# Optimization experiments

Measured on AMD Instinct MI355X. Metric: run time of the kernel, lower is better.

Reference implementation:

```python
import jax, jax.numpy as jnp
import numpy as np


def setup_inputs() -> dict:
    key = jax.random.key(0)
    ks = jax.random.split(key, 11)
    B, T, H1, H2 = 256, 512, 1024, 1024
    s1 = 1.0 / np.sqrt(H1)
    s2 = 1.0 / np.sqrt(H2)
    return {
        "x": jax.random.normal(ks[0], (B, 2, T), dtype=jnp.float32),
        "W_ih1": jax.random.normal(ks[1], (H1, 2), dtype=jnp.float32) * s1,
        "W_hh1": jax.random.normal(ks[2], (H1, H1), dtype=jnp.float32) * s1,
        "b_ih1": jax.random.normal(ks[3], (H1,), dtype=jnp.float32) * s1,
        "b_hh1": jax.random.normal(ks[4], (H1,), dtype=jnp.float32) * s1,
        "W_ih2": jax.random.normal(ks[5], (H2, H1), dtype=jnp.float32) * s2,
        "W_hh2": jax.random.normal(ks[6], (H2, H2), dtype=jnp.float32) * s2,
        "b_ih2": jax.random.normal(ks[7], (H2,), dtype=jnp.float32) * s2,
        "b_hh2": jax.random.normal(ks[8], (H2,), dtype=jnp.float32) * s2,
        "W_lin": jax.random.normal(ks[9], (2, H2), dtype=jnp.float32) * s2,
        "b_lin": jax.random.normal(ks[10], (2,), dtype=jnp.float32) * s2,
        "future": 0,
    }


def _run(x, W_ih1, W_hh1, b_ih1, b_hh1, W_ih2, W_hh2, b_ih2, b_hh2, W_lin, b_lin, future):
    # x: [B, 2, T]  -> scan over time with xs [T, B, 2]
    B = x.shape[0]
    H1, H2 = W_hh1.shape[0], W_hh2.shape[0]

    def cell(x_t, h1, h2):
        # torch RNNCell (tanh): h' = tanh(x W_ih^T + b_ih + h W_hh^T + b_hh)
        h1 = jnp.tanh(x_t @ W_ih1.T + b_ih1 + h1 @ W_hh1.T + b_hh1)
        h2 = jnp.tanh(h1 @ W_ih2.T + b_ih2 + h2 @ W_hh2.T + b_hh2)
        out = h2 @ W_lin.T + b_lin  # [B, 2]
        return h1, h2, out

    def step(carry, x_t):
        h1, h2 = carry
        h1, h2, out = cell(x_t, h1, h2)
        return (h1, h2), out

    h1 = jnp.zeros((B, H1), dtype=x.dtype)
    h2 = jnp.zeros((B, H2), dtype=x.dtype)
    xs = jnp.transpose(x, (2, 0, 1))  # [T, B, 2]
    (h1, h2), outs = jax.lax.scan(step, (h1, h2), xs)  # outs: [T, B, 2]

    if future > 0:
        last = outs[-1]

        def fstep(carry, _):
            h1, h2, out = carry
            h1, h2, out = cell(out, h1, h2)
            return (h1, h2, out), out

        _, fouts = jax.lax.scan(fstep, (h1, h2, last), None, length=future)
        outs = jnp.concatenate([outs, fouts], axis=0)

    return jnp.transpose(outs, (1, 2, 0))  # [B, 2, T+future]


def reference(x, W_ih1, W_hh1, b_ih1, b_hh1, W_ih2, W_hh2, b_ih2, b_hh2, W_lin, b_lin, future):
    return _run(x, W_ih1, W_hh1, b_ih1, b_hh1, W_ih2, W_hh2, b_ih2, b_hh2, W_lin, b_lin, future)
```

## Files before the change

### kernel.cpp

```cpp
#include <hip/hip_runtime.h>

#define NB 256
#define NT 512
#define NH 1024
#define BH (NB * NH)
#define GRID_WGS 256
#define BLOCK 512

typedef __attribute__((ext_vector_type(8))) __bf16 bfrag;
typedef __attribute__((ext_vector_type(4))) float f32x4;
typedef __attribute__((ext_vector_type(4))) unsigned u32x4;
typedef __attribute__((ext_vector_type(8))) unsigned short u16x8;
typedef unsigned short us;

__device__ __attribute__((aligned(16))) us g_h1[3 * BH];
__device__ __attribute__((aligned(16))) us g_h2[4 * BH];
__device__ __attribute__((aligned(128))) unsigned g_flagA[GRID_WGS];
__device__ __attribute__((aligned(128))) unsigned g_flagB[GRID_WGS];

__device__ __forceinline__ us f2bf(float f) {
  union { float f; unsigned u; } v; v.f = f;
  unsigned r = v.u + 0x7FFFu + ((v.u >> 16) & 1u);
  return (us)(r >> 16);
}
__device__ __forceinline__ float bf2f(us u) {
  union { unsigned u; float f; } v; v.u = ((unsigned)u) << 16;
  return v.f;
}

__device__ __forceinline__ bfrag cvt8(const float* __restrict__ p) {
  f32x4 a = *reinterpret_cast<const f32x4*>(p);
  f32x4 b = *reinterpret_cast<const f32x4*>(p + 4);
  u16x8 u;
#pragma unroll
  for (int i = 0; i < 4; ++i) { u[i] = f2bf(a[i]); u[i + 4] = f2bf(b[i]); }
  union { u16x8 u; bfrag b; } c; c.u = u; return c.b;
}

union f16u { u32x4 v; bfrag b; u16x8 s; };
__device__ __forceinline__ u32x4 ld16_dev(const void* p) {
  u32x4 r;
  asm volatile("global_load_dwordx4 %0, %1, off sc0 sc1" : "=v"(r) : "v"(p));
  return r;
}
__device__ __forceinline__ unsigned ld4_dev(const void* p) {
  unsigned r;
  asm volatile("global_load_dword %0, %1, off sc0 sc1\n\ts_waitcnt vmcnt(0)"
               : "=v"(r) : "v"(p) : "memory");
  return r;
}
__device__ __forceinline__ void st4_dev(void* p, unsigned v) {
  asm volatile("global_store_dword %0, %1, off sc0 sc1" :: "v"(p), "v"(v) : "memory");
}

__device__ __forceinline__ void wait4(const unsigned* f, int lane, unsigned tgt) {
  unsigned v = tgt;
  for (;;) {
    if (lane < 4) v = ld4_dev(f + lane);
    if (!__any((int)(v < tgt))) break;
    __builtin_amdgcn_s_sleep(1);
  }
}
__device__ __forceinline__ void wait32(const unsigned* f, int lane, unsigned tgt) {
  unsigned v = tgt;
  for (;;) {
    if (lane < 32) v = ld4_dev(f + lane);
    if (!__any((int)(v < tgt))) break;
    __builtin_amdgcn_s_sleep(1);
  }
}

__device__ __forceinline__ void out_row(const us* h2, int r_g, int w, int lane,
                                        const float* __restrict__ Wlin,
                                        const float* __restrict__ blin,
                                        float* __restrict__ out, int t) {
  const us* hp = h2 + r_g * NH + lane * 16;
  const float* wl = Wlin + w * NH + lane * 16;
  f16u h0, h1v;
  h0.v  = ld16_dev(hp);
  h1v.v = ld16_dev(hp + 8);
  asm volatile("s_waitcnt vmcnt(0)" ::: "memory");
  __builtin_amdgcn_sched_barrier(0);
  float s = 0.f;
#pragma unroll
  for (int e = 0; e < 8; ++e) {
    s = fmaf(bf2f(h0.s[e]),  wl[e],     s);
    s = fmaf(bf2f(h1v.s[e]), wl[8 + e], s);
  }
#pragma unroll
  for (int m = 1; m < 64; m <<= 1) s += __shfl_xor(s, m);
  if (lane == 0) out[r_g * (2 * NT) + w * NT + t] = s + blin[w];
}

#define MFMA(a, b, c) __builtin_amdgcn_mfma_f32_16x16x32_bf16((a), (b), (c), 0, 0, 0)

__global__ void __launch_bounds__(BLOCK, 1) rnn_kernel(
    const float* __restrict__ x,
    const float* __restrict__ Wi1,
    const float* __restrict__ Whh1,
    const float* __restrict__ Wih2,
    const float* __restrict__ Whh2,
    const float* __restrict__ bih1,
    const float* __restrict__ bhh1,
    const float* __restrict__ bih2,
    const float* __restrict__ bhh2,
    const float* __restrict__ Wlin,
    const float* __restrict__ blin,
    float* __restrict__ out)
{
  const int bid = blockIdx.x, tid = threadIdx.x;
  const int w = tid >> 6, lane = tid & 63;
  const int mb = bid >> 5, nb = bid & 31;
  unsigned* gfA = g_flagA + mb * 32;
  unsigned* gfB = g_flagB + mb * 32;

  const unsigned fbA = ld4_dev(&gfA[nb]);
  const unsigned fbB = ld4_dev(&gfB[nb]);

  {
    const int zrow = tid >> 4, zc = tid & 15;
    const int off_d = ((mb * 32 + zrow) * NH + nb * 32) / 2;
    st4_dev((unsigned*)(g_h1 + 2 * BH) + off_d + zc, 0u);
    st4_dev((unsigned*)(g_h2 + 2 * BH) + off_d + zc, 0u);
    st4_dev((unsigned*)(g_h2 + 3 * BH) + off_d + zc, 0u);
  }

  const int fr = lane & 15;
  const int ko = (lane >> 4) << 3;
  const int kbase = w * 128;
  bfrag w1[2][4], w2i[2][4], w2h[2][4];
#pragma unroll
  for (int cf = 0; cf < 2; ++cf)
#pragma unroll
    for (int st = 0; st < 4; ++st) {
      const int off = (nb * 32 + cf * 16 + fr) * NH + kbase + st * 32 + ko;
      w1[cf][st]  = cvt8(Whh1 + off);
      w2i[cf][st] = cvt8(Wih2 + off);
      w2h[cf][st] = cvt8(Whh2 + off);
    }

  const int rl = tid >> 4, cl = (tid & 15) * 2;
  const int grow = mb * 32 + rl, gcol = nb * 32 + cl;
  const float b1s0 = bih1[gcol] + bhh1[gcol];
  const float b1s1 = bih1[gcol + 1] + bhh1[gcol + 1];
  const float b2s0 = bih2[gcol] + bhh2[gcol];
  const float b2s1 = bih2[gcol + 1] + bhh2[gcol + 1];
  const float wi00 = Wi1[gcol * 2],       wi01 = Wi1[gcol * 2 + 1];
  const float wi10 = Wi1[(gcol + 1) * 2], wi11 = Wi1[(gcol + 1) * 2 + 1];
  const float* xrow = x + grow * (2 * NT);

  __shared__ float redA[8][32][36];
  __shared__ float redB[8][32][36];

  const int arow0 = mb * 32 + fr;
  const int prow = (lane >> 4) << 2;
  const int r_g = bid;

  asm volatile("s_waitcnt vmcnt(0)" ::: "memory");
  __syncthreads();
  if (tid == 0) { st4_dev(&gfA[nb], fbA + 1u); st4_dev(&gfB[nb], fbB + 1u); }

  for (int p = 0; p <= NT; ++p) {
    const us* h1_prev = g_h1 + ((p + 2) % 3) * BH;
    us*       h1_cur  = g_h1 + (p % 3) * BH;
    const us* h2_pp   = g_h2 + ((p + 2) & 3) * BH;
    us*       h2_cur  = g_h2 + ((p + 3) & 3) * BH;
    const us* h2_out  = g_h2 + ((p + 1) & 3) * BH;

    wait4(gfA + w * 4, lane, fbA + 1u + (unsigned)p);
    __builtin_amdgcn_sched_barrier(0);

    const float x0 = xrow[p < NT ? p : 0], x1 = xrow[NT + (p < NT ? p : 0)];

    f16u a1[2][4];
    {
      const us* pa = h1_prev + arow0 * NH + kbase + ko;
      const us* pb = h1_prev + (arow0 + 16) * NH + kbase + ko;
#pragma unroll
      for (int st = 0; st < 4; ++st) a1[0][st].v = ld16_dev(pa + st * 32);
#pragma unroll
      for (int st = 0; st < 4; ++st) a1[1][st].v = ld16_dev(pb + st * 32);
    }
    f32x4 accA[2][2] = {};
    asm volatile("s_waitcnt vmcnt(4)" ::: "memory");
    __builtin_amdgcn_sched_barrier(0);
#pragma unroll
    for (int st = 0; st < 4; ++st) {
      accA[0][0] = MFMA(a1[0][st].b, w1[0][st], accA[0][0]);
      accA[0][1] = MFMA(a1[0][st].b, w1[1][st], accA[0][1]);
    }
    asm volatile("s_waitcnt vmcnt(0)" ::: "memory");
    __builtin_amdgcn_sched_barrier(0);
#pragma unroll
    for (int st = 0; st < 4; ++st) {
      accA[1][0] = MFMA(a1[1][st].b, w1[0][st], accA[1][0]);
      accA[1][1] = MFMA(a1[1][st].b, w1[1][st], accA[1][1]);
    }
#pragma unroll
    for (int mf = 0; mf < 2; ++mf)
#pragma unroll
      for (int cf = 0; cf < 2; ++cf)
#pragma unroll
        for (int r = 0; r < 4; ++r)
          redA[w][mf * 16 + prow + r][cf * 16 + fr] = accA[mf][cf][r];
    __syncthreads();

    if (p < NT) {
      float sA0 = 0.f, sA1 = 0.f;
#pragma unroll
      for (int u = 0; u < 8; ++u) {
        const float2 a = *reinterpret_cast<const float2*>(&redA[u][rl][cl]);
        sA0 += a.x; sA1 += a.y;
      }
      const float v0 = sA0 + b1s0 + x0 * wi00 + x1 * wi01;
      const float v1 = sA1 + b1s1 + x0 * wi10 + x1 * wi11;
      st4_dev(h1_cur + grow * NH + gcol,
              (unsigned)f2bf(tanhf(v0)) | ((unsigned)f2bf(tanhf(v1)) << 16));
    }
    asm volatile("s_waitcnt vmcnt(0)" ::: "memory");
    __syncthreads();
    if (tid == 0) st4_dev(&gfA[nb], fbA + 2u + (unsigned)p);

    if (p >= 3 && w < 2)
      out_row(h2_out, r_g, w, lane, Wlin, blin, out, p - 3);

    if (p >= 2) wait4(gfB + w * 4, lane, fbB + (unsigned)p);
    __builtin_amdgcn_sched_barrier(0);

    f16u a2[2][4];
    {
      const us* pa = h2_pp + arow0 * NH + kbase + ko;
      const us* pb = h2_pp + (arow0 + 16) * NH + kbase + ko;
#pragma unroll
      for (int st = 0; st < 4; ++st) a2[0][st].v = ld16_dev(pa + st * 32);
#pragma unroll
      for (int st = 0; st < 4; ++st) a2[1][st].v = ld16_dev(pb + st * 32);
    }
    f32x4 accB[2][2] = {};
    asm volatile("s_waitcnt vmcnt(4)" ::: "memory");
    __builtin_amdgcn_sched_barrier(0);
#pragma unroll
    for (int st = 0; st < 4; ++st) {
      accB[0][0] = MFMA(a1[0][st].b, w2i[0][st], accB[0][0]);
      accB[0][1] = MFMA(a1[0][st].b, w2i[1][st], accB[0][1]);
      accB[0][0] = MFMA(a2[0][st].b, w2h[0][st], accB[0][0]);
      accB[0][1] = MFMA(a2[0][st].b, w2h[1][st], accB[0][1]);
    }
    asm volatile("s_waitcnt vmcnt(0)" ::: "memory");
    __builtin_amdgcn_sched_barrier(0);
#pragma unroll
    for (int st = 0; st < 4; ++st) {
      accB[1][0] = MFMA(a1[1][st].b, w2i[0][st], accB[1][0]);
      accB[1][1] = MFMA(a1[1][st].b, w2i[1][st], accB[1][1]);
      accB[1][0] = MFMA(a2[1][st].b, w2h[0][st], accB[1][0]);
      accB[1][1] = MFMA(a2[1][st].b, w2h[1][st], accB[1][1]);
    }
#pragma unroll
    for (int mf = 0; mf < 2; ++mf)
#pragma unroll
      for (int cf = 0; cf < 2; ++cf)
#pragma unroll
        for (int r = 0; r < 4; ++r)
          redB[w][mf * 16 + prow + r][cf * 16 + fr] = accB[mf][cf][r];
    __syncthreads();

    if (p >= 1) {
      float sB0 = 0.f, sB1 = 0.f;
#pragma unroll
      for (int u = 0; u < 8; ++u) {
        const float2 b = *reinterpret_cast<const float2*>(&redB[u][rl][cl]);
        sB0 += b.x; sB1 += b.y;
      }
      const float v0 = sB0 + b2s0;
      const float v1 = sB1 + b2s1;
      st4_dev(h2_cur + grow * NH + gcol,
              (unsigned)f2bf(tanhf(v0)) | ((unsigned)f2bf(tanhf(v1)) << 16));
    }
    asm volatile("s_waitcnt vmcnt(0)" ::: "memory");
    __syncthreads();
    if (tid == 0) st4_dev(&gfB[nb], fbB + 1u + (unsigned)p);
  }

  wait32(gfB, lane, fbB + 1u + (unsigned)NT);
  if (w < 2) {
    out_row(g_h2 + ((NT - 2) & 3) * BH, r_g, w, lane, Wlin, blin, out, NT - 2);
    out_row(g_h2 + ((NT - 1) & 3) * BH, r_g, w, lane, Wlin, blin, out, NT - 1);
  }
}

extern "C" void kernel_launch(void* const* d_in, const int* in_sizes, int n_in,
                              void* d_out, int out_size, void* d_ws, size_t ws_size,
                              hipStream_t stream) {
  (void)in_sizes; (void)n_in; (void)d_ws; (void)ws_size; (void)out_size;
  const float* x    = (const float*)d_in[0];
  const float* Wi1  = (const float*)d_in[1];
  const float* Whh1 = (const float*)d_in[2];
  const float* bih1 = (const float*)d_in[3];
  const float* bhh1 = (const float*)d_in[4];
  const float* Wih2 = (const float*)d_in[5];
  const float* Whh2 = (const float*)d_in[6];
  const float* bih2 = (const float*)d_in[7];
  const float* bhh2 = (const float*)d_in[8];
  const float* Wlin = (const float*)d_in[9];
  const float* blin = (const float*)d_in[10];
  float* out = (float*)d_out;

  void* args[] = { (void*)&x, (void*)&Wi1, (void*)&Whh1, (void*)&Wih2, (void*)&Whh2,
                   (void*)&bih1, (void*)&bhh1, (void*)&bih2, (void*)&bhh2,
                   (void*)&Wlin, (void*)&blin, (void*)&out };
  hipLaunchCooperativeKernel((void*)rnn_kernel, dim3(GRID_WGS), dim3(BLOCK),
                             args, 0, stream);
}
```

Measured before the change: 3.858 ms.

## Merge layer-1 and layer-2 phases into one wavefront-synchronized step per iteration

Layer-1 and layer-2 recurrent GEMMs, which previously ran as two barrier- and flag-separated phases, are now fused into one phase per time step under a single global flag per workgroup. The h1 ring buffer grows to four slots, and the shared-memory reduction buffers are double-buffered by parity so the trailing __syncthreads can be dropped. The flag is now published by the last wave to increment an LDS atomic counter. The output projection loads its h2 row alongside the GEMM operands, and the Wlin weights are preloaded into registers. The aim is to halve the grid-wide handshakes and barriers per step, at the cost of a longer dependency chain and more register pressure per step.

```diff
diff --git a/kernel.cpp b/kernel.cpp
--- a/kernel.cpp
+++ b/kernel.cpp
@@ -6,6 +6,7 @@
 #define BH (NB * NH)
 #define GRID_WGS 256
 #define BLOCK 512
+#define T2 (2 * NT)
 
 typedef __attribute__((ext_vector_type(8))) __bf16 bfrag;
 typedef __attribute__((ext_vector_type(4))) float f32x4;
@@ -13,10 +14,9 @@
 typedef __attribute__((ext_vector_type(8))) unsigned short u16x8;
 typedef unsigned short us;
 
-__device__ __attribute__((aligned(16))) us g_h1[3 * BH];
+__device__ __attribute__((aligned(16))) us g_h1[4 * BH];
 __device__ __attribute__((aligned(16))) us g_h2[4 * BH];
-__device__ __attribute__((aligned(128))) unsigned g_flagA[GRID_WGS];
-__device__ __attribute__((aligned(128))) unsigned g_flagB[GRID_WGS];
+__device__ __attribute__((aligned(128))) unsigned g_flag[GRID_WGS];
 
 __device__ __forceinline__ us f2bf(float f) {
   union { float f; unsigned u; } v; v.f = f;
@@ -27,7 +27,6 @@
   union { unsigned u; float f; } v; v.u = ((unsigned)u) << 16;
   return v.f;
 }
-
 __device__ __forceinline__ bfrag cvt8(const float* __restrict__ p) {
   f32x4 a = *reinterpret_cast<const f32x4*>(p);
   f32x4 b = *reinterpret_cast<const f32x4*>(p + 4);
@@ -70,29 +69,12 @@
   }
 }
 
-__device__ __forceinline__ void out_row(const us* h2, int r_g, int w, int lane,
-                                        const float* __restrict__ Wlin,
-                                        const float* __restrict__ blin,
-                                        float* __restrict__ out, int t) {
-  const us* hp = h2 + r_g * NH + lane * 16;
-  const float* wl = Wlin + w * NH + lane * 16;
-  f16u h0, h1v;
-  h0.v  = ld16_dev(hp);
-  h1v.v = ld16_dev(hp + 8);
-  asm volatile("s_waitcnt vmcnt(0)" ::: "memory");
-  __builtin_amdgcn_sched_barrier(0);
-  float s = 0.f;
-#pragma unroll
-  for (int e = 0; e < 8; ++e) {
-    s = fmaf(bf2f(h0.s[e]),  wl[e],     s);
-    s = fmaf(bf2f(h1v.s[e]), wl[8 + e], s);
-  }
-#pragma unroll
-  for (int m = 1; m < 64; m <<= 1) s += __shfl_xor(s, m);
-  if (lane == 0) out[r_g * (2 * NT) + w * NT + t] = s + blin[w];
+__device__ __forceinline__ unsigned cadd(unsigned* c) {
+  return __hip_atomic_fetch_add(c, 1u, __ATOMIC_RELAXED, __HIP_MEMORY_SCOPE_WORKGROUP);
 }
 
 #define MFMA(a, b, c) __builtin_amdgcn_mfma_f32_16x16x32_bf16((a), (b), (c), 0, 0, 0)
+#define SB() __builtin_amdgcn_sched_barrier(0)
 
 __global__ void __launch_bounds__(BLOCK, 1) rnn_kernel(
     const float* __restrict__ x,
@@ -111,18 +93,20 @@
   const int bid = blockIdx.x, tid = threadIdx.x;
   const int w = tid >> 6, lane = tid & 63;
   const int mb = bid >> 5, nb = bid & 31;
-  unsigned* gfA = g_flagA + mb * 32;
-  unsigned* gfB = g_flagB + mb * 32;
-
-  const unsigned fbA = ld4_dev(&gfA[nb]);
-  const unsigned fbB = ld4_dev(&gfB[nb]);
+  unsigned* gf = g_flag + mb * 32;
+  const unsigned fb = ld4_dev(&gf[nb]);
+
+  __shared__ float redA[2][8][32][36];
+  __shared__ float redB[2][8][32][36];
+  __shared__ unsigned s_cnt;
+  if (tid == 0) s_cnt = 0;
 
   {
     const int zrow = tid >> 4, zc = tid & 15;
-    const int off_d = ((mb * 32 + zrow) * NH + nb * 32) / 2;
-    st4_dev((unsigned*)(g_h1 + 2 * BH) + off_d + zc, 0u);
-    st4_dev((unsigned*)(g_h2 + 2 * BH) + off_d + zc, 0u);
-    st4_dev((unsigned*)(g_h2 + 3 * BH) + off_d + zc, 0u);
+    const int off_d = ((mb * 32 + zrow) * NH + nb * 32) / 2 + zc;
+    st4_dev((unsigned*)(g_h1 + 3 * BH) + off_d, 0u);
+    st4_dev((unsigned*)(g_h2 + 2 * BH) + off_d, 0u);
+    st4_dev((unsigned*)(g_h2 + 3 * BH) + off_d, 0u);
   }
 
   const int fr = lane & 15;
@@ -147,144 +131,152 @@
   const float b2s1 = bih2[gcol + 1] + bhh2[gcol + 1];
   const float wi00 = Wi1[gcol * 2],       wi01 = Wi1[gcol * 2 + 1];
   const float wi10 = Wi1[(gcol + 1) * 2], wi11 = Wi1[(gcol + 1) * 2 + 1];
-  const float* xrow = x + grow * (2 * NT);
-
-  __shared__ float redA[8][32][36];
-  __shared__ float redB[8][32][36];
+  const float* xrow = x + grow * T2;
 
   const int arow0 = mb * 32 + fr;
   const int prow = (lane >> 4) << 2;
   const int r_g = bid;
 
+  float wl[16]; float blc = 0.f;
+  if (w < 2) {
+#pragma unroll
+    for (int j = 0; j < 16; ++j) wl[j] = Wlin[w * NH + lane * 16 + j];
+    blc = blin[w];
+  }
+
   asm volatile("s_waitcnt vmcnt(0)" ::: "memory");
   __syncthreads();
-  if (tid == 0) { st4_dev(&gfA[nb], fbA + 1u); st4_dev(&gfB[nb], fbB + 1u); }
+  if (tid == 0) st4_dev(&gf[nb], fb + 1u);
 
   for (int p = 0; p <= NT; ++p) {
-    const us* h1_prev = g_h1 + ((p + 2) % 3) * BH;
-    us*       h1_cur  = g_h1 + (p % 3) * BH;
+    const int par = p & 1;
+    const us* h1_prev = g_h1 + ((p + 3) & 3) * BH;
+    us*       h1_cur  = g_h1 + (p & 3) * BH;
     const us* h2_pp   = g_h2 + ((p + 2) & 3) * BH;
     us*       h2_cur  = g_h2 + ((p + 3) & 3) * BH;
     const us* h2_out  = g_h2 + ((p + 1) & 3) * BH;
 
-    wait4(gfA + w * 4, lane, fbA + 1u + (unsigned)p);
-    __builtin_amdgcn_sched_barrier(0);
-
-    const float x0 = xrow[p < NT ? p : 0], x1 = xrow[NT + (p < NT ? p : 0)];
-
-    f16u a1[2][4];
+    const int px = (p < NT) ? p : 0;
+    const float x0 = xrow[px], x1 = xrow[NT + px];
+
+    wait4(gf + w * 4, lane, fb + 1u + (unsigned)p);
+    SB();
+
+    f16u o0, o1, a1[2][4], a2[2][4];
+    const int do_out = (w < 2) && (p >= 3);
+    if (do_out) {
+      o0.v = ld16_dev(h2_out + r_g * NH + lane * 16);
+      o1.v = ld16_dev(h2_out + r_g * NH + lane * 16 + 8);
+    }
     {
-      const us* pa = h1_prev + arow0 * NH + kbase + ko;
-      const us* pb = h1_prev + (arow0 + 16) * NH + kbase + ko;
-#pragma unroll
-      for (int st = 0; st < 4; ++st) a1[0][st].v = ld16_dev(pa + st * 32);
-#pragma unroll
-      for (int st = 0; st < 4; ++st) a1[1][st].v = ld16_dev(pb + st * 32);
-    }
-    f32x4 accA[2][2] = {};
-    asm volatile("s_waitcnt vmcnt(4)" ::: "memory");
-    __builtin_amdgcn_sched_barrier(0);
+      const us* pa0 = h1_prev + arow0 * NH + kbase + ko;
+      const us* pa1 = h1_prev + (arow0 + 16) * NH + kbase + ko;
+#pragma unroll
+      for (int st = 0; st < 4; ++st) a1[0][st].v = ld16_dev(pa0 + st * 32);
+#pragma unroll
+      for (int st = 0; st < 4; ++st) a1[1][st].v = ld16_dev(pa1 + st * 32);
+      const us* pb0 = h2_pp + arow0 * NH + kbase + ko;
+      const us* pb1 = h2_pp + (arow0 + 16) * NH + kbase + ko;
+#pragma unroll
+      for (int st = 0; st < 4; ++st) a2[0][st].v = ld16_dev(pb0 + st * 32);
+#pragma unroll
+      for (int st = 0; st < 4; ++st) a2[1][st].v = ld16_dev(pb1 + st * 32);
+    }
+
+    f32x4 accA[2][2] = {}; f32x4 accB[2][2] = {};
+    asm volatile("s_waitcnt vmcnt(8)" ::: "memory");
+    SB();
 #pragma unroll
     for (int st = 0; st < 4; ++st) {
-      accA[0][0] = MFMA(a1[0][st].b, w1[0][st], accA[0][0]);
-      accA[0][1] = MFMA(a1[0][st].b, w1[1][st], accA[0][1]);
+      accA[0][0] = MFMA(a1[0][st].b, w1[0][st],  accA[0][0]);
+      accA[0][1] = MFMA(a1[0][st].b, w1[1][st],  accA[0][1]);
+      accA[1][0] = MFMA(a1[1][st].b, w1[0][st],  accA[1][0]);
+      accA[1][1] = MFMA(a1[1][st].b, w1[1][st],  accA[1][1]);
+      accB[0][0] = MFMA(a1[0][st].b, w2i[0][st], accB[0][0]);
+      accB[0][1] = MFMA(a1[0][st].b, w2i[1][st], accB[0][1]);
+      accB[1][0] = MFMA(a1[1][st].b, w2i[0][st], accB[1][0]);
+      accB[1][1] = MFMA(a1[1][st].b, w2i[1][st], accB[1][1]);
     }
     asm volatile("s_waitcnt vmcnt(0)" ::: "memory");
-    __builtin_amdgcn_sched_barrier(0);
+    SB();
 #pragma unroll
     for (int st = 0; st < 4; ++st) {
-      accA[1][0] = MFMA(a1[1][st].b, w1[0][st], accA[1][0]);
-      accA[1][1] = MFMA(a1[1][st].b, w1[1][st], accA[1][1]);
-    }
+      accB[0][0] = MFMA(a2[0][st].b, w2h[0][st], accB[0][0]);
+      accB[0][1] = MFMA(a2[0][st].b, w2h[1][st], accB[0][1]);
+      accB[1][0] = MFMA(a2[1][st].b, w2h[0][st], accB[1][0]);
+      accB[1][1] = MFMA(a2[1][st].b, w2h[1][st], accB[1][1]);
+    }
+
 #pragma unroll
     for (int mf = 0; mf < 2; ++mf)
 #pragma unroll
       for (int cf = 0; cf < 2; ++cf)
 #pragma unroll
-        for (int r = 0; r < 4; ++r)
-          redA[w][mf * 16 + prow + r][cf * 16 + fr] = accA[mf][cf][r];
+        for (int r = 0; r < 4; ++r) {
+          redA[par][w][mf * 16 + prow + r][cf * 16 + fr] = accA[mf][cf][r];
+          redB[par][w][mf * 16 + prow + r][cf * 16 + fr] = accB[mf][cf][r];
+        }
     __syncthreads();
 
+    float sA0 = 0.f, sA1 = 0.f, sB0 = 0.f, sB1 = 0.f;
+#pragma unroll
+    for (int u = 0; u < 8; ++u) {
+      const float2 a = *reinterpret_cast<const float2*>(&redA[par][u][rl][cl]);
+      const float2 b = *reinterpret_cast<const float2*>(&redB[par][u][rl][cl]);
+      sA0 += a.x; sA1 += a.y; sB0 += b.x; sB1 += b.y;
+    }
     if (p < NT) {
-      float sA0 = 0.f, sA1 = 0.f;
-#pragma unroll
-      for (int u = 0; u < 8; ++u) {
-        const float2 a = *reinterpret_cast<const float2*>(&redA[u][rl][cl]);
-        sA0 += a.x; sA1 += a.y;
-      }
       const float v0 = sA0 + b1s0 + x0 * wi00 + x1 * wi01;
       const float v1 = sA1 + b1s1 + x0 * wi10 + x1 * wi11;
       st4_dev(h1_cur + grow * NH + gcol,
               (unsigned)f2bf(tanhf(v0)) | ((unsigned)f2bf(tanhf(v1)) << 16));
     }
-    asm volatile("s_waitcnt vmcnt(0)" ::: "memory");
-    __syncthreads();
-    if (tid == 0) st4_dev(&gfA[nb], fbA + 2u + (unsigned)p);
-
-    if (p >= 3 && w < 2)
-      out_row(h2_out, r_g, w, lane, Wlin, blin, out, p - 3);
-
-    if (p >= 2) wait4(gfB + w * 4, lane, fbB + (unsigned)p);
-    __builtin_amdgcn_sched_barrier(0);
-
-    f16u a2[2][4];
-    {
-      const us* pa = h2_pp + arow0 * NH + kbase + ko;
-      const us* pb = h2_pp + (arow0 + 16) * NH + kbase + ko;
-#pragma unroll
-      for (int st = 0; st < 4; ++st) a2[0][st].v = ld16_dev(pa + st * 32);
-#pragma unroll
-      for (int st = 0; st < 4; ++st) a2[1][st].v = ld16_dev(pb + st * 32);
-    }
-    f32x4 accB[2][2] = {};
-    asm volatile("s_waitcnt vmcnt(4)" ::: "memory");
-    __builtin_amdgcn_sched_barrier(0);
-#pragma unroll
-    for (int st = 0; st < 4; ++st) {
-      accB[0][0] = MFMA(a1[0][st].b, w2i[0][st], accB[0][0]);
-      accB[0][1] = MFMA(a1[0][st].b, w2i[1][st], accB[0][1]);
-      accB[0][0] = MFMA(a2[0][st].b, w2h[0][st], accB[0][0]);
-      accB[0][1] = MFMA(a2[0][st].b, w2h[1][st], accB[0][1]);
-    }
-    asm volatile("s_waitcnt vmcnt(0)" ::: "memory");
-    __builtin_amdgcn_sched_barrier(0);
-#pragma unroll
-    for (int st = 0; st < 4; ++st) {
-      accB[1][0] = MFMA(a1[1][st].b, w2i[0][st], accB[1][0]);
-      accB[1][1] = MFMA(a1[1][st].b, w2i[1][st], accB[1][1]);
-      accB[1][0] = MFMA(a2[1][st].b, w2h[0][st], accB[1][0]);
-      accB[1][1] = MFMA(a2[1][st].b, w2h[1][st], accB[1][1]);
-    }
-#pragma unroll
-    for (int mf = 0; mf < 2; ++mf)
-#pragma unroll
-      for (int cf = 0; cf < 2; ++cf)
-#pragma unroll
-        for (int r = 0; r < 4; ++r)
-          redB[w][mf * 16 + prow + r][cf * 16 + fr] = accB[mf][cf][r];
-    __syncthreads();
-
     if (p >= 1) {
-      float sB0 = 0.f, sB1 = 0.f;
-#pragma unroll
-      for (int u = 0; u < 8; ++u) {
-        const float2 b = *reinterpret_cast<const float2*>(&redB[u][rl][cl]);
-        sB0 += b.x; sB1 += b.y;
-      }
       const float v0 = sB0 + b2s0;
       const float v1 = sB1 + b2s1;
       st4_dev(h2_cur + grow * NH + gcol,
               (unsigned)f2bf(tanhf(v0)) | ((unsigned)f2bf(tanhf(v1)) << 16));
     }
+
     asm volatile("s_waitcnt vmcnt(0)" ::: "memory");
-    __syncthreads();
-    if (tid == 0) st4_dev(&gfB[nb], fbB + 1u + (unsigned)p);
-  }
-
-  wait32(gfB, lane, fbB + 1u + (unsigned)NT);
+    if (lane == 0) {
+      const unsigned old = cadd(&s_cnt);
+      if (old == 8u * (unsigned)p + 7u) st4_dev(&gf[nb], fb + 2u + (unsigned)p);
+    }
+
+    if (do_out) {
+      float so = 0.f;
+#pragma unroll
+      for (int e = 0; e < 8; ++e) {
+        so = fmaf(bf2f(o0.s[e]), wl[e],     so);
+        so = fmaf(bf2f(o1.s[e]), wl[8 + e], so);
+      }
+#pragma unroll
+      for (int m = 1; m < 64; m <<= 1) so += __shfl_xor(so, m);
+      if (lane == 0) out[r_g * T2 + w * NT + (p - 3)] = so + blc;
+    }
+  }
+
+  wait32(gf, lane, fb + 2u + (unsigned)NT);
   if (w < 2) {
-    out_row(g_h2 + ((NT - 2) & 3) * BH, r_g, w, lane, Wlin, blin, out, NT - 2);
-    out_row(g_h2 + ((NT - 1) & 3) * BH, r_g, w, lane, Wlin, blin, out, NT - 1);
+#pragma unroll
+    for (int t = NT - 2; t < NT; ++t) {
+      const us* h2t = g_h2 + (t & 3) * BH;
+      f16u o0, o1;
+      o0.v = ld16_dev(h2t + r_g * NH + lane * 16);
+      o1.v = ld16_dev(h2t + r_g * NH + lane * 16 + 8);
+      asm volatile("s_waitcnt vmcnt(0)" ::: "memory");
+      SB();
+      float so = 0.f;
+#pragma unroll
+      for (int e = 0; e < 8; ++e) {
+        so = fmaf(bf2f(o0.s[e]), wl[e],     so);
+        so = fmaf(bf2f(o1.s[e]), wl[8 + e], so);
+      }
+#pragma unroll
+      for (int m = 1; m < 64; m <<= 1) so += __shfl_xor(so, m);
+      if (lane == 0) out[r_g * T2 + w * NT + t] = so + blc;
+    }
   }
 }
 
```

Result: slower. 3.977 ms (+3.1%).
